# Kernel tuning notes

Hardware: AMD Instinct MI355X
Metric: run time of the kernel (lower is better)

Reference implementation:

```python
import jax, jax.numpy as jnp
import numpy as np

N = 25000      # nodes
E = 300000     # edges
IN = 32        # in_dim
EDF = 16       # edge_feat_dim
HID = 256      # hidden_dim (per-head dim, concat=False)
HEADS = 4
ACT = 16       # num_actions
G = 64         # graphs in batch
KW = 1024      # wire-mask query nodes


def setup_inputs() -> dict:
    key = jax.random.key(0)
    ks = jax.random.split(key, 20)
    def rn(k, shape, s=0.1):
        return jax.random.normal(k, shape, jnp.float32) * s
    return {
        "x": jax.random.normal(ks[0], (N, IN), jnp.float32),
        "edge_attr": jax.random.normal(ks[1], (E, EDF), jnp.float32),
        "wire_mask": jax.random.randint(ks[2], (KW,), 0, N, jnp.int32),
        "edge_index": jax.random.randint(ks[3], (2, E), 0, N, jnp.int32),
        "batch": jnp.sort(jax.random.randint(ks[4], (N,), 0, G, jnp.int32)),
        "enc_w1": rn(ks[5], (EDF, 32)),
        "enc_b1": jnp.zeros((32,), jnp.float32),
        "enc_w2": rn(ks[6], (32, IN * IN), 0.05),
        "enc_b2": jnp.zeros((IN * IN,), jnp.float32),
        "root_w": rn(ks[7], (IN, IN)),
        "nn_bias": jnp.zeros((IN,), jnp.float32),
        "gat1_w": rn(ks[8], (IN, HEADS * HID)),
        "gat1_asrc": rn(ks[9], (HEADS, HID)),
        "gat1_adst": rn(ks[10], (HEADS, HID)),
        "gat1_b": jnp.zeros((HID,), jnp.float32),
        "gat2_w": rn(ks[11], (HID, HEADS * HID)),
        "gat2_asrc": rn(ks[12], (HEADS, HID)),
        "gat2_adst": rn(ks[13], (HEADS, HID)),
        "gat2_b": jnp.zeros((HID,), jnp.float32),
        "wire_w": rn(ks[14], (HID, 1)),
        "wire_b": jnp.zeros((1,), jnp.float32),
        "act_w": rn(ks[15], (HID, ACT)),
        "act_b": jnp.zeros((ACT,), jnp.float32),
    }


def _gat(x, src, dst, W, a_src, a_dst, b):
    # PyG GATConv, concat=False (mean over heads), eval mode (no dropout),
    # self-loops already included in (src, dst).
    H, D = a_src.shape
    h = (x @ W).reshape(-1, H, D)                      # [N, H, D]
    es = (h * a_src[None]).sum(-1)                     # [N, H]
    ed = (h * a_dst[None]).sum(-1)                     # [N, H]
    e = jax.nn.leaky_relu(es[src] + ed[dst], negative_slope=0.2)  # [E2, H]
    m = jax.ops.segment_max(e, dst, num_segments=N)    # segment softmax (stable)
    w = jnp.exp(e - m[dst])
    den = jax.ops.segment_sum(w, dst, num_segments=N)
    alpha = w / (den[dst] + 1e-16)
    out = jax.ops.segment_sum(h[src] * alpha[..., None], dst, num_segments=N)
    return out.mean(axis=1) + b                        # [N, D]


def reference(x, edge_attr, wire_mask, edge_index, batch,
              enc_w1, enc_b1, enc_w2, enc_b2, root_w, nn_bias,
              gat1_w, gat1_asrc, gat1_adst, gat1_b,
              gat2_w, gat2_asrc, gat2_adst, gat2_b,
              wire_w, wire_b, act_w, act_b):
    src, dst = edge_index[0], edge_index[1]
    # NNConv (aggr='mean'): per-edge weight matrix from edge MLP
    We = (jax.nn.relu(edge_attr @ enc_w1 + enc_b1) @ enc_w2 + enc_b2)
    We = We.reshape(E, IN, IN)                         # [E, in, out]
    msg = jnp.einsum('ei,eio->eo', x[src], We)         # [E, out]
    s = jax.ops.segment_sum(msg, dst, num_segments=N)
    cnt = jax.ops.segment_sum(jnp.ones((E,), x.dtype), dst, num_segments=N)
    agg = s / jnp.maximum(cnt, 1.0)[:, None]
    h0 = jax.nn.relu(agg + x @ root_w + nn_bias)
    # GATConv default add_self_loops=True
    sl = jnp.arange(N, dtype=src.dtype)
    src2 = jnp.concatenate([src, sl])
    dst2 = jnp.concatenate([dst, sl])
    h1 = jax.nn.relu(_gat(h0, src2, dst2, gat1_w, gat1_asrc, gat1_adst, gat1_b))
    h2 = jax.nn.relu(_gat(h1, src2, dst2, gat2_w, gat2_asrc, gat2_adst, gat2_b))
    p_wire = (h2[wire_mask] @ wire_w + wire_b).squeeze(-1)   # [KW]
    pooled_s = jax.ops.segment_sum(h2, batch, num_segments=G)
    gc = jax.ops.segment_sum(jnp.ones((N,), h2.dtype), batch, num_segments=G)
    pooled = pooled_s / jnp.maximum(gc, 1.0)[:, None]        # global_mean_pool
    p_action = pooled @ act_w + act_b                        # [G, ACT]
    return (p_wire, p_action)
```

## Files before the change

### kernel.cpp

```cpp
#include <hip/hip_runtime.h>
#include <hip/hip_fp16.h>

#define N_NODES 25000
#define M_PAD   25024
#define N_TILES 1564
#define N_EDGES 300000
#define IN_DIM  32
#define EDFD    16
#define HIDD    256
#define HEADS   4
#define NACT    16
#define NGRAPH  64
#define KWIRE   1024
#define POOL_NB 64

typedef _Float16 half8v __attribute__((ext_vector_type(8)));
typedef __attribute__((ext_vector_type(4))) float f32x4;

__device__ __forceinline__ float leaky(float v) { return v > 0.f ? v : 0.2f * v; }

__global__ __launch_bounds__(256) void k_deg2(const int* __restrict__ ei,
                                              int* __restrict__ deg,
                                              int* __restrict__ deg2) {
    int e = blockIdx.x * 256 + threadIdx.x;
    if (e >= N_EDGES) return;
    atomicAdd(&deg[ei[N_EDGES + e]], 1);
    atomicAdd(&deg2[ei[e]], 1);
}

__global__ __launch_bounds__(256) void k_scan2(const int* __restrict__ degA, int* __restrict__ rpA,
                                               const int* __restrict__ degB, int* __restrict__ rpB) {
    const int* deg = blockIdx.x ? degB : degA;
    int* rowptr    = blockIdx.x ? rpB : rpA;
    __shared__ int part[256];
    int t = threadIdx.x;
    const int CH = 98;
    int base = t * CH;
    int s = 0;
    for (int i = 0; i < CH; ++i) {
        int idx = base + i;
        if (idx < N_NODES) s += deg[idx];
    }
    part[t] = s;
    __syncthreads();
    if (t == 0) {
        int run = 0;
        for (int i = 0; i < 256; ++i) { int v = part[i]; part[i] = run; run += v; }
    }
    __syncthreads();
    int run = part[t];
    for (int i = 0; i < CH; ++i) {
        int idx = base + i;
        if (idx < N_NODES) { rowptr[idx] = run; run += deg[idx]; }
    }
    if (N_NODES >= base && N_NODES < base + CH) rowptr[N_NODES] = run;
}

__global__ __launch_bounds__(256) void k_scatter2(const int* __restrict__ ei,
                                                  const float* __restrict__ ea,
                                                  const int* __restrict__ rowptr,
                                                  const int* __restrict__ rowptr2,
                                                  int* __restrict__ cursor,
                                                  int* __restrict__ cursor2,
                                                  int* __restrict__ csrc,
                                                  int* __restrict__ cdst,
                                                  int* __restrict__ posMap,
                                                  __half* __restrict__ eaP) {
    int e = blockIdx.x * 256 + threadIdx.x;
    if (e >= N_EDGES) return;
    int src = ei[e], dst = ei[N_EDGES + e];
    int p1 = atomicAdd(&cursor[dst], 1);
    int r1 = rowptr[dst] + p1;
    csrc[r1] = src;
    int p2 = atomicAdd(&cursor2[src], 1);
    int r2 = rowptr2[src] + p2;
    cdst[r2] = dst;
    posMap[r2] = r1;
    const float4* src4 = (const float4*)(ea + (size_t)e * EDFD);
    __half2* dp = (__half2*)(eaP + (size_t)r2 * EDFD);
    #pragma unroll
    for (int q = 0; q < EDFD / 4; ++q) {
        float4 v = src4[q];
        dp[q * 2]     = __float22half2_rn(make_float2(v.x, v.y));
        dp[q * 2 + 1] = __float22half2_rn(make_float2(v.z, v.w));
    }
}

__global__ __launch_bounds__(256) void k_prep(const float* __restrict__ w2,
                                              const float* __restrict__ W1,
                                              const float* __restrict__ W2,
                                              const float* __restrict__ a1s,
                                              const float* __restrict__ a1d,
                                              const float* __restrict__ a2s,
                                              const float* __restrict__ a2d,
                                              const float* __restrict__ x,
                                              const float* __restrict__ b2,
                                              const float* __restrict__ w1,
                                              __half* __restrict__ wtt,
                                              __half* __restrict__ wb1,
                                              __half* __restrict__ wb2,
                                              float* __restrict__ wa1,
                                              float* __restrict__ wd1,
                                              float* __restrict__ wa2,
                                              float* __restrict__ wd2,
                                              __half* __restrict__ xf,
                                              float* __restrict__ xb,
                                              __half* __restrict__ w1t) {
    int bid = blockIdx.x, t = threadIdx.x;
    if (bid < 128) {
        int idx = bid * 256 + t;
        int co = idx >> 5, i = idx & 31;
        wtt[idx] = __float2half(w2[(co >> 5) * 1024 + i * 32 + (co & 31)]);
    } else if (bid < 256) {
        int idx = (bid - 128) * 256 + t;
        int d = idx >> 7, k = idx & 127;
        int h = k >> 5, i = k & 31;
        wb1[idx] = __float2half(0.25f * W1[i * 1024 + h * 256 + d]);
    } else if (bid < 1280) {
        int idx = (bid - 256) * 256 + t;
        int d = idx >> 10, k = idx & 1023;
        int h = k >> 8, i = k & 255;
        wb2[idx] = __float2half(0.25f * W2[i * 1024 + h * 256 + d]);
    } else if (bid < 4405) {
        int idx = (bid - 1280) * 256 + t;
        if (idx >= N_NODES * 32) return;
        int n = idx >> 5, o = idx & 31;
        xf[idx] = __float2half(x[idx]);
        float s = 0.f;
        for (int i = 0; i < 32; ++i) s += x[n * 32 + i] * b2[i * 32 + o];
        xb[idx] = s;
    } else if (bid == 4405) {
        if (t >= 128) return;
        int h = t >> 5, i = t & 31;
        float s = 0.f, sd = 0.f;
        for (int d = 0; d < 256; ++d) {
            float w = W1[i * 1024 + h * 256 + d];
            s  += w * a1s[h * 256 + d];
            sd += w * a1d[h * 256 + d];
        }
        wa1[t] = s; wd1[t] = sd;
    } else if (bid < 4410) {
        int idx = (bid - 4406) * 256 + t;
        if (idx >= 1024) return;
        int h = idx >> 8, i = idx & 255;
        float s = 0.f, sd = 0.f;
        for (int d = 0; d < 256; ++d) {
            float w = W2[i * 1024 + h * 256 + d];
            s  += w * a2s[h * 256 + d];
            sd += w * a2d[h * 256 + d];
        }
        wa2[idx] = s; wd2[idx] = sd;
    } else {
        int idx = (bid - 4410) * 256 + t;
        if (idx >= 32 * EDFD) return;
        int j = idx >> 4, k = idx & 15;
        w1t[idx] = __float2half(w1[k * 32 + j]);
    }
}

__global__ __launch_bounds__(256) void k_msg3(const int* __restrict__ rowptr2,
                                              const int* __restrict__ posMap,
                                              const __half* __restrict__ eaP,
                                              const __half* __restrict__ w1t,
                                              const float* __restrict__ b1,
                                              const __half* __restrict__ T,
                                              const float* __restrict__ xb,
                                              __half* __restrict__ msgE) {
    int wv = threadIdx.x >> 6, lane = threadIdx.x & 63;
    int src = blockIdx.x * 4 + wv;
    if (src >= N_NODES) return;
    int r0 = rowptr2[src], r1 = rowptr2[src + 1];
    if (r0 == r1) return;
    int lr = lane & 15, lk = (lane >> 4) * 8;

    half8v bf0, bf1;
    const __half* Tp = T + (size_t)src * 1024;
    #pragma unroll
    for (int q = 0; q < 8; ++q) {
        bf0[q] = (_Float16)__half2float(Tp[(lk + q) * 32 + lr]);
        bf1[q] = (_Float16)__half2float(Tp[(lk + q) * 32 + 16 + lr]);
    }

    __half2 w1r[8][EDFD / 2];
    #pragma unroll
    for (int q = 0; q < 8; ++q) {
        const __half2* wp = (const __half2*)(w1t + (lk + q) * EDFD);
        #pragma unroll
        for (int k2 = 0; k2 < EDFD / 2; ++k2) w1r[q][k2] = wp[k2];
    }
    float b1r[8];
    #pragma unroll
    for (int q = 0; q < 8; ++q) b1r[q] = b1[lk + q];

    float xb0 = xb[src * 32 + lr], xb1 = xb[src * 32 + 16 + lr];
    int rbase = (lane >> 4) * 4;

    for (int t0 = r0; t0 < r1; t0 += 16) {
        int e = t0 + lr;
        bool ok = (e < r1);
        half8v afr;
        if (ok) {
            const __half2* ep = (const __half2*)(eaP + (size_t)e * EDFD);
            __half2 ea2[EDFD / 2];
            #pragma unroll
            for (int k2 = 0; k2 < EDFD / 2; ++k2) ea2[k2] = ep[k2];
            #pragma unroll
            for (int q = 0; q < 8; ++q) {
                float s = b1r[q];
                #pragma unroll
                for (int k2 = 0; k2 < EDFD / 2; ++k2) {
                    float2 v = __half22float2(ea2[k2]);
                    float2 w = __half22float2(w1r[q][k2]);
                    s += v.x * w.x + v.y * w.y;
                }
                afr[q] = (_Float16)fmaxf(s, 0.f);
            }
        } else {
            #pragma unroll
            for (int q = 0; q < 8; ++q) afr[q] = (_Float16)0.f;
        }
        f32x4 c0 = {0.f, 0.f, 0.f, 0.f}, c1 = {0.f, 0.f, 0.f, 0.f};
        c0 = __builtin_amdgcn_mfma_f32_16x16x32_f16(afr, bf0, c0, 0, 0, 0);
        c1 = __builtin_amdgcn_mfma_f32_16x16x32_f16(afr, bf1, c1, 0, 0, 0);
        #pragma unroll
        for (int r = 0; r < 4; ++r) {
            int er = t0 + rbase + r;
            if (er < r1) {
                int pm = posMap[er];
                msgE[(size_t)pm * 32 + lr]      = __float2half(c0[r] + xb0);
                msgE[(size_t)pm * 32 + 16 + lr] = __float2half(c1[r] + xb1);
            }
        }
    }
}

__global__ __launch_bounds__(256) void k_h0e(const float* __restrict__ x,
                                             const float* __restrict__ root_w,
                                             const float* __restrict__ nn_bias,
                                             const __half* __restrict__ msgE,
                                             const int* __restrict__ rowptr,
                                             const float* __restrict__ wa,
                                             const float* __restrict__ wd,
                                             __half* __restrict__ h0f,
                                             float* __restrict__ es,
                                             float* __restrict__ ed) {
    int t = threadIdx.x;
    int ng = t >> 5, o = t & 31;
    int n = blockIdx.x * 8 + ng;
    if (n >= N_NODES) return;
    float s = nn_bias[o];
    for (int k = 0; k < IN_DIM; ++k) s += x[n * IN_DIM + k] * root_w[k * 32 + o];
    int r0 = rowptr[n], r1 = rowptr[n + 1];
    float aggv = 0.f;
    for (int r = r0; r < r1; ++r)
        aggv += __half2float(msgE[(size_t)r * 32 + o]);
    float c = fmaxf((float)(r1 - r0), 1.f);
    s += aggv / c;
    float v = fmaxf(s, 0.f);
    h0f[n * IN_DIM + o] = __float2half(v);
    #pragma unroll
    for (int h = 0; h < 4; ++h) {
        float ss = v * wa[h * 32 + o];
        float dd = v * wd[h * 32 + o];
        #pragma unroll
        for (int off = 16; off; off >>= 1) {
            ss += __shfl_down(ss, off, 32);
            dd += __shfl_down(dd, off, 32);
        }
        if (o == 0) { es[n * 4 + h] = ss; ed[n * 4 + h] = dd; }
    }
}

__global__ __launch_bounds__(256, 2) void k_gemT(const __half* __restrict__ A,
                                                 const __half* __restrict__ Wt,
                                                 __half* __restrict__ C) {
    __shared__ __half cst[4][16 * 36];
    int t = threadIdx.x, wid = t >> 6, lane = t & 63;
    int lr = lane & 15, lk = (lane >> 4) * 8;

    int bid = blockIdx.x;
    int xcd = bid & 7, j = bid >> 3;
    int sx = j & 31;
    int y = ((j >> 5) << 3) | xcd;
    int n0 = sx * 32;

    half8v bfr[2];
    #pragma unroll
    for (int c = 0; c < 2; ++c)
        bfr[c] = *(const half8v*)(Wt + (size_t)(n0 + c * 16 + lr) * 32 + lk);

    int tb = (y * 4 + wid) * 4;
    for (int pp = 0; pp < 4; pp += 2) {
        int tA = tb + pp;
        if (tA >= N_TILES) break;
        int mA = tA * 16, mB = mA + 16;
        half8v aA = *(const half8v*)(A + (size_t)(mA + lr) * 32 + lk);
        half8v aB = *(const half8v*)(A + (size_t)(mB + lr) * 32 + lk);
        f32x4 acc[2][2];
        #pragma unroll
        for (int i = 0; i < 2; ++i)
            #pragma unroll
            for (int c = 0; c < 2; ++c)
                acc[i][c] = (f32x4){0.f, 0.f, 0.f, 0.f};
        acc[0][0] = __builtin_amdgcn_mfma_f32_16x16x32_f16(aA, bfr[0], acc[0][0], 0, 0, 0);
        acc[0][1] = __builtin_amdgcn_mfma_f32_16x16x32_f16(aA, bfr[1], acc[0][1], 0, 0, 0);
        acc[1][0] = __builtin_amdgcn_mfma_f32_16x16x32_f16(aB, bfr[0], acc[1][0], 0, 0, 0);
        acc[1][1] = __builtin_amdgcn_mfma_f32_16x16x32_f16(aB, bfr[1], acc[1][1], 0, 0, 0);

        int rbase = (lane >> 4) * 4;
        #pragma unroll
        for (int ti = 0; ti < 2; ++ti) {
            #pragma unroll
            for (int c = 0; c < 2; ++c)
                #pragma unroll
                for (int r = 0; r < 4; ++r)
                    cst[wid][(rbase + r) * 36 + c * 16 + lr] = __float2half(acc[ti][c][r]);
            int m0 = ti ? mB : mA;
            #pragma unroll
            for (int p = 0; p < 2; ++p) {
                int row = p * 8 + (lane >> 3), hb = lane & 7;
                float2 v = *(const float2*)((const char*)&cst[wid][0] + row * 72 + hb * 8);
                *(float2*)((char*)C + ((size_t)(m0 + row) * 1024 + n0) * 2 + hb * 8) = v;
            }
        }
    }
}

template <int K, typename OT, bool FUSE_ED>
__global__ __launch_bounds__(256, 3) void k_gemmo(const __half* __restrict__ A,
                                                  const __half* __restrict__ Wt,
                                                  const float* __restrict__ bias,
                                                  OT* __restrict__ C,
                                                  const float* __restrict__ wa,
                                                  const float* __restrict__ wd,
                                                  float* __restrict__ es,
                                                  float* __restrict__ ed) {
    constexpr int CK  = 128;
    constexpr int KC  = K / CK;
    constexpr int KSC = CK / 32;
    constexpr int CB  = CK * 2;
    __shared__ __half bs[2][64 * CK];
    __shared__ float cst[4][16 * 36];
    int t = threadIdx.x, wid = t >> 6, lane = t & 63;
    int lr = lane & 15, lk = (lane >> 4) * 8;

    int bid = blockIdx.x;
    int xcd = bid & 7, rest = bid >> 3;
    int strip = rest & 3, yhi = rest >> 2;
    int y = yhi * 8 + xcd;
    if (y >= 196) return;
    int n0 = strip * 64;
    float bv[4];
    #pragma unroll
    for (int c = 0; c < 4; ++c) bv[c] = bias[n0 + c * 16 + lr];
    int tb = y * 8 + wid * 2;
    int tA0 = tb     < N_TILES ? tb     : N_TILES - 1;
    int tA1 = tb + 1 < N_TILES ? tb + 1 : N_TILES - 1;
    const int swz = (lr & 7) << 4;

    f32x4 acc[2][4];
    #pragma unroll
    for (int i = 0; i < 2; ++i)
        #pragma unroll
        for (int c = 0; c < 4; ++c)
            acc[i][c] = (f32x4){0.f, 0.f, 0.f, 0.f};

    #define STAGE_CHUNK(BUF, KCN)                                                              \
        _Pragma("unroll")                                                                      \
        for (int it = 0; it < (64 * CB) / (256 * 16); ++it) {                                  \
            int lo = it * 4096 + wid * 1024 + lane * 16;                                       \
            int col = lo >> 8;                                                                 \
            int go = lo ^ ((col & 7) << 4);                                                    \
            const char* sp_ = (const char*)Wt + ((size_t)(n0 + col) * K + (KCN) * CK) * 2      \
                              + (go & (CB - 1));                                               \
            __builtin_amdgcn_global_load_lds(                                                  \
                (const __attribute__((address_space(1))) void*)sp_,                            \
                (__attribute__((address_space(3))) void*)((char*)bs[BUF] + it * 4096 + wid * 1024), \
                16, 0, 0);                                                                     \
        }

    STAGE_CHUNK(0, 0)
    __syncthreads();

    const __half* pA0 = A + (size_t)(tA0 * 16 + lr) * K + lk;
    const __half* pA1 = A + (size_t)(tA1 * 16 + lr) * K + lk;

    for (int kc = 0; kc < KC; ++kc) {
        int cur = kc & 1;
        if (kc + 1 < KC) {
            STAGE_CHUNK(cur ^ 1, kc + 1)
        }
        half8v aH0[KSC], aH1[KSC];
        #pragma unroll
        for (int ks = 0; ks < KSC; ++ks) {
            aH0[ks] = *(const half8v*)(pA0 + kc * CK + ks * 32);
            aH1[ks] = *(const half8v*)(pA1 + kc * CK + ks * 32);
        }
        #pragma unroll
        for (int ks = 0; ks < KSC; ++ks) {
            #pragma unroll
            for (int c = 0; c < 4; ++c) {
                half8v b = *(const half8v*)((const char*)bs[cur] +
                            (((c * 16 + lr) * CB + lk * 2 + ks * 64) ^ swz));
                acc[0][c] = __builtin_amdgcn_mfma_f32_16x16x32_f16(aH0[ks], b, acc[0][c], 0, 0, 0);
                acc[1][c] = __builtin_amdgcn_mfma_f32_16x16x32_f16(aH1[ks], b, acc[1][c], 0, 0, 0);
            }
        }
        if (kc + 1 < KC) __syncthreads();
    }
    #undef STAGE_CHUNK

    int rbase = (lane >> 4) * 4;
    #pragma unroll
    for (int ti = 0; ti < 2; ++ti) {
        if (tb + ti >= N_TILES) break;
        int m0 = (tb + ti) * 16;
        int row = lane >> 2, cg = lane & 3;
        #pragma unroll
        for (int half = 0; half < 2; ++half) {
            #pragma unroll
            for (int c = 0; c < 2; ++c)
                #pragma unroll
                for (int r = 0; r < 4; ++r)
                    cst[wid][(rbase + r) * 36 + c * 16 + lr] =
                        fmaxf(acc[ti][half * 2 + c][r] + bv[half * 2 + c], 0.f);
            int colb = n0 + half * 32;
            const float* sp = &cst[wid][row * 36 + cg * 8];
            if constexpr (sizeof(OT) == 2) {
                __half2 o0 = __float22half2_rn(make_float2(sp[0], sp[1]));
                __half2 o1 = __float22half2_rn(make_float2(sp[2], sp[3]));
                __half2 o2 = __float22half2_rn(make_float2(sp[4], sp[5]));
                __half2 o3 = __float22half2_rn(make_float2(sp[6], sp[7]));
                float4 v = make_float4(__uint_as_float(*(unsigned*)&o0), __uint_as_float(*(unsigned*)&o1),
                                       __uint_as_float(*(unsigned*)&o2), __uint_as_float(*(unsigned*)&o3));
                *(float4*)((__half*)C + (size_t)(m0 + row) * 256 + colb + cg * 8) = v;
            } else {
                float4 v0 = make_float4(sp[0], sp[1], sp[2], sp[3]);
                float4 v1 = make_float4(sp[4], sp[5], sp[6], sp[7]);
                float* cp = (float*)C + (size_t)(m0 + row) * 256 + colb + cg * 8;
                *(float4*)cp = v0;
                *(float4*)(cp + 4) = v1;
            }
            if constexpr (FUSE_ED) {
                int rowg = m0 + row;
                #pragma unroll
                for (int h = 0; h < 4; ++h) {
                    float pes = 0.f, ped = 0.f;
                    #pragma unroll
                    for (int d = 0; d < 8; ++d) {
                        float vv = sp[d];
                        pes += vv * wa[h * 256 + colb + cg * 8 + d];
                        ped += vv * wd[h * 256 + colb + cg * 8 + d];
                    }
                    pes += __shfl_down(pes, 1, 4); pes += __shfl_down(pes, 2, 4);
                    ped += __shfl_down(ped, 1, 4); ped += __shfl_down(ped, 2, 4);
                    if (cg == 0 && rowg < N_NODES) {
                        atomicAdd(&es[rowg * 4 + h], pes);
                        atomicAdd(&ed[rowg * 4 + h], ped);
                    }
                }
            }
        }
    }
}

__global__ __launch_bounds__(256) void k_agg1(const int* __restrict__ rowptr,
                                              const int* __restrict__ csrc,
                                              const float* __restrict__ es,
                                              const float* __restrict__ ed,
                                              const __half* __restrict__ h0f,
                                              __half* __restrict__ agg0) {
    int dst = blockIdx.x * 4 + (threadIdx.x >> 6);
    if (dst >= N_NODES) return;
    int lane = threadIdx.x & 63;
    int h = lane >> 4, i2 = lane & 15;
    float edv = ed[dst * 4 + h];
    float vself = leaky(es[dst * 4 + h] + edv);
    float dn = 1.f;
    int r0 = rowptr[dst], r1 = rowptr[dst + 1];

    __half2 hv = *(const __half2*)(h0f + (size_t)dst * 32 + i2 * 2);
    float2 f = __half22float2(hv);
    float ax = f.x, ay = f.y;
    for (int r = r0; r < r1; ++r) {
        int src = csrc[r];
        float w = __expf(leaky(es[src * 4 + h] + edv) - vself);
        dn += w;
        __half2 sv = *(const __half2*)(h0f + (size_t)src * 32 + i2 * 2);
        float2 g = __half22float2(sv);
        ax += w * g.x; ay += w * g.y;
    }
    float inv = 1.f / (dn + 1e-16f);
    *(__half2*)(agg0 + (size_t)dst * 128 + h * 32 + i2 * 2) =
        __float22half2_rn(make_float2(ax * inv, ay * inv));
}

__global__ __launch_bounds__(256) void k_agg2(const int* __restrict__ rowptr,
                                              const int* __restrict__ csrc,
                                              const float* __restrict__ es,
                                              const float* __restrict__ ed,
                                              const __half* __restrict__ h1f,
                                              __half* __restrict__ agg1) {
    int dst = blockIdx.x * 4 + (threadIdx.x >> 6);
    if (dst >= N_NODES) return;
    int lane = threadIdx.x & 63;
    float vs[4], edv[4], dn[4];
    float acc[4][4];
    {
        float2 q = *(const float2*)(h1f + (size_t)dst * 256 + lane * 4);
        const __half2* hq = (const __half2*)&q;
        float2 f0 = __half22float2(hq[0]), f1 = __half22float2(hq[1]);
        #pragma unroll
        for (int h = 0; h < 4; ++h) {
            edv[h] = ed[dst * 4 + h];
            vs[h] = leaky(es[dst * 4 + h] + edv[h]);
            dn[h] = 1.f;
            acc[h][0] = f0.x; acc[h][1] = f0.y;
            acc[h][2] = f1.x; acc[h][3] = f1.y;
        }
    }
    int r0 = rowptr[dst], r1 = rowptr[dst + 1];
    for (int r = r0; r < r1; ++r) {
        int src = csrc[r];
        float4 esv = *(const float4*)(es + (size_t)src * 4);
        float w0 = __expf(leaky(esv.x + edv[0]) - vs[0]);
        float w1 = __expf(leaky(esv.y + edv[1]) - vs[1]);
        float w2 = __expf(leaky(esv.z + edv[2]) - vs[2]);
        float w3 = __expf(leaky(esv.w + edv[3]) - vs[3]);
        dn[0] += w0; dn[1] += w1; dn[2] += w2; dn[3] += w3;
        float2 q = *(const float2*)(h1f + (size_t)src * 256 + lane * 4);
        const __half2* hq = (const __half2*)&q;
        float2 f0 = __half22float2(hq[0]), f1 = __half22float2(hq[1]);
        acc[0][0] += w0 * f0.x; acc[0][1] += w0 * f0.y; acc[0][2] += w0 * f1.x; acc[0][3] += w0 * f1.y;
        acc[1][0] += w1 * f0.x; acc[1][1] += w1 * f0.y; acc[1][2] += w1 * f1.x; acc[1][3] += w1 * f1.y;
        acc[2][0] += w2 * f0.x; acc[2][1] += w2 * f0.y; acc[2][2] += w2 * f1.x; acc[2][3] += w2 * f1.y;
        acc[3][0] += w3 * f0.x; acc[3][1] += w3 * f0.y; acc[3][2] += w3 * f1.x; acc[3][3] += w3 * f1.y;
    }
    #pragma unroll
    for (int h = 0; h < 4; ++h) {
        float inv = 1.f / (dn[h] + 1e-16f);
        __half2 o0 = __float22half2_rn(make_float2(acc[h][0] * inv, acc[h][1] * inv));
        __half2 o1 = __float22half2_rn(make_float2(acc[h][2] * inv, acc[h][3] * inv));
        __half2* op = (__half2*)(agg1 + (size_t)dst * 1024 + h * 256 + lane * 4);
        op[0] = o0; op[1] = o1;
    }
}

__global__ __launch_bounds__(256) void k_wirepool(const int* __restrict__ wm,
                                                  const float* __restrict__ h2,
                                                  const float* __restrict__ ww,
                                                  const float* __restrict__ wb,
                                                  const int* __restrict__ batch,
                                                  float* __restrict__ out,
                                                  float* __restrict__ pooled,
                                                  float* __restrict__ gcnt) {
    int bid = blockIdx.x;
    if (bid < KWIRE / 4) {
        int k = bid * 4 + (threadIdx.x >> 6);
        int lane = threadIdx.x & 63;
        int n = wm[k];
        float s = 0.f;
        for (int d = lane; d < 256; d += 64) s += h2[(size_t)n * 256 + d] * ww[d];
        #pragma unroll
        for (int off = 32; off; off >>= 1) s += __shfl_down(s, off);
        if (lane == 0) out[k] = s + wb[0];
        return;
    }
    int n0 = (bid - KWIRE / 4) * POOL_NB;
    int n1 = n0 + POOL_NB; if (n1 > N_NODES) n1 = N_NODES;
    int d = threadIdx.x;
    int cur = batch[n0];
    float acc = 0.f, cnt = 0.f;
    for (int n = n0; n < n1; ++n) {
        int g = batch[n];
        if (g != cur) {
            atomicAdd(&pooled[cur * 256 + d], acc);
            if (d == 0) atomicAdd(&gcnt[cur], cnt);
            acc = 0.f; cnt = 0.f; cur = g;
        }
        acc += h2[(size_t)n * 256 + d];
        cnt += 1.f;
    }
    atomicAdd(&pooled[cur * 256 + d], acc);
    if (d == 0) atomicAdd(&gcnt[cur], cnt);
}

__global__ __launch_bounds__(256) void k_act(const float* __restrict__ pooled,
                                             const float* __restrict__ gcnt,
                                             const float* __restrict__ aw,
                                             const float* __restrict__ ab,
                                             float* __restrict__ out) {
    int u = blockIdx.x * 4 + (threadIdx.x >> 6);
    int lane = threadIdx.x & 63;
    if (u >= NGRAPH * NACT) return;
    int g = u >> 4, a = u & 15;
    float c = fmaxf(gcnt[g], 1.f);
    float s = 0.f;
    for (int d = lane; d < 256; d += 64) s += pooled[g * 256 + d] * aw[d * 16 + a];
    #pragma unroll
    for (int off = 32; off; off >>= 1) s += __shfl_down(s, off);
    if (lane == 0) out[KWIRE + u] = s / c + ab[a];
}

extern "C" void kernel_launch(void* const* d_in, const int* in_sizes, int n_in,
                              void* d_out, int out_size, void* d_ws, size_t ws_size,
                              hipStream_t stream) {
    const float* x        = (const float*)d_in[0];
    const float* edge_attr= (const float*)d_in[1];
    const int*   wire_mask= (const int*)d_in[2];
    const int*   edge_idx = (const int*)d_in[3];
    const int*   batch    = (const int*)d_in[4];
    const float* enc_w1   = (const float*)d_in[5];
    const float* enc_b1   = (const float*)d_in[6];
    const float* enc_w2   = (const float*)d_in[7];
    const float* enc_b2   = (const float*)d_in[8];
    const float* root_w   = (const float*)d_in[9];
    const float* nn_bias  = (const float*)d_in[10];
    const float* gat1_w   = (const float*)d_in[11];
    const float* gat1_asrc= (const float*)d_in[12];
    const float* gat1_adst= (const float*)d_in[13];
    const float* gat1_b   = (const float*)d_in[14];
    const float* gat2_w   = (const float*)d_in[15];
    const float* gat2_asrc= (const float*)d_in[16];
    const float* gat2_adst= (const float*)d_in[17];
    const float* gat2_b   = (const float*)d_in[18];
    const float* wire_w   = (const float*)d_in[19];
    const float* wire_b   = (const float*)d_in[20];
    const float* act_w    = (const float*)d_in[21];
    const float* act_b    = (const float*)d_in[22];
    float* out = (float*)d_out;

    float* ws = (float*)d_ws;
    size_t off = 0;
    __half* T16   = (__half*)(ws + off); off += (size_t)M_PAD * 1024 / 2;
    __half* agg1f = (__half*)(ws + off); off += (size_t)M_PAD * 1024 / 2;
    __half* agg0f = (__half*)(ws + off); off += (size_t)M_PAD * 128 / 2;
    __half* h0f   = (__half*)(ws + off); off += (size_t)M_PAD * 32 / 2;
    __half* h1f   = (__half*)(ws + off); off += (size_t)M_PAD * 256 / 2;
    __half* xf    = (__half*)(ws + off); off += (size_t)M_PAD * 32 / 2;
    __half* eaP   = (__half*)(ws + off); off += (size_t)N_EDGES * EDFD / 2;
    __half* msgE  = (__half*)(ws + off); off += (size_t)N_EDGES * 32 / 2;
    float* xb     = ws + off; off += 800000;
    float* esb    = ws + off; off += 100000;
    float* edb    = ws + off; off += 100000;
    float* h2     = ws + off; off += (size_t)M_PAD * 256;
    float* pooled = ws + off; off += NGRAPH * 256;
    float* gcnt   = ws + off; off += NGRAPH;
    int* deg      = (int*)(ws + off); off += 25600;
    int* deg2     = (int*)(ws + off); off += 25600;
    int* cursor   = (int*)(ws + off); off += 25600;
    int* cursor2  = (int*)(ws + off); off += 25600;
    int* rowptr   = (int*)(ws + off); off += 25600;
    int* rowptr2  = (int*)(ws + off); off += 25600;
    int* csrc     = (int*)(ws + off); off += N_EDGES;
    int* cdst     = (int*)(ws + off); off += N_EDGES;
    int* posMap   = (int*)(ws + off); off += N_EDGES;
    __half* wtt   = (__half*)(ws + off); off += 16384;
    __half* wb1t  = (__half*)(ws + off); off += 16384;
    __half* wb2t  = (__half*)(ws + off); off += 131072;
    __half* w1t   = (__half*)(ws + off); off += 256;
    float* wa1    = ws + off; off += 128;
    float* wd1    = ws + off; off += 128;
    float* wa2    = ws + off; off += 1024;
    float* wd2    = ws + off; off += 1024;
    float* esb2   = ws + off; off += 100000;
    float* edb2   = ws + off; off += 100000;

    const int GBT = 3328;
    const int GBO = 800;

    hipMemsetAsync(deg, 0, 4 * 25600 * sizeof(int), stream);
    hipMemsetAsync(esb2, 0, 2 * 100000 * sizeof(float), stream);
    k_deg2<<<(N_EDGES + 255) / 256, 256, 0, stream>>>(edge_idx, deg, deg2);
    k_scan2<<<2, 256, 0, stream>>>(deg, rowptr, deg2, rowptr2);
    k_scatter2<<<(N_EDGES + 255) / 256, 256, 0, stream>>>(edge_idx, edge_attr, rowptr, rowptr2,
                                                          cursor, cursor2, csrc, cdst, posMap, eaP);

    k_prep<<<4412, 256, 0, stream>>>(enc_w2, gat1_w, gat2_w, gat1_asrc, gat1_adst,
                                     gat2_asrc, gat2_adst, x, enc_b2, enc_w1,
                                     wtt, wb1t, wb2t, wa1, wd1, wa2, wd2, xf, xb, w1t);

    k_gemT<<<GBT, 256, 0, stream>>>(xf, wtt, T16);
    k_msg3<<<(N_NODES + 3) / 4, 256, 0, stream>>>(rowptr2, posMap, eaP,
                                                  w1t, enc_b1, T16, xb, msgE);
    k_h0e<<<(N_NODES + 7) / 8, 256, 0, stream>>>(x, root_w, nn_bias, msgE, rowptr,
                                                 wa1, wd1, h0f, esb, edb);

    k_agg1<<<(N_NODES + 3) / 4, 256, 0, stream>>>(rowptr, csrc, esb, edb, h0f, agg0f);
    k_gemmo<128, __half, true><<<GBO, 256, 0, stream>>>(agg0f, wb1t, gat1_b, h1f,
                                                        wa2, wd2, esb2, edb2);

    k_agg2<<<(N_NODES + 3) / 4, 256, 0, stream>>>(rowptr, csrc, esb2, edb2, h1f, agg1f);
    k_gemmo<1024, float, false><<<GBO, 256, 0, stream>>>(agg1f, wb2t, gat2_b, h2,
                                                         nullptr, nullptr, nullptr, nullptr);

    hipMemsetAsync(pooled, 0, (NGRAPH * 256 + NGRAPH) * sizeof(float), stream);
    k_wirepool<<<KWIRE / 4 + (N_NODES + POOL_NB - 1) / POOL_NB, 256, 0, stream>>>(
        wire_mask, h2, wire_w, wire_b, batch, out, pooled, gcnt);
    k_act<<<NGRAPH * NACT / 4, 256, 0, stream>>>(pooled, gcnt, act_w, act_b, out);
}
```

Measured before the change: 412.7 us.

## Precompute GAT attention weights per edge in a separate kernel before aggregation

Adds a k_wgt kernel that computes the exponentiated attention weight for every (edge, head) once and stores it along with the inverse softmax denominator. The aggregation kernels then read these precomputed weights instead of recomputing exp/leaky-relu redundantly in every lane of a wave. The cost is an extra kernel launch per GAT layer, a 4.8 MB weight buffer write and read, and a weight-computing kernel with one thread per (node, head) that walks irregular-length rows.

```diff
diff --git a/kernel.cpp b/kernel.cpp
--- a/kernel.cpp
+++ b/kernel.cpp
@@ -464,19 +464,37 @@
     }
 }
 
+__global__ __launch_bounds__(256) void k_wgt(const int* __restrict__ rowptr,
+                                             const int* __restrict__ csrc,
+                                             const float* __restrict__ es,
+                                             const float* __restrict__ ed,
+                                             float* __restrict__ wgt,
+                                             float* __restrict__ invdn) {
+    int u = blockIdx.x * 256 + threadIdx.x;
+    if (u >= N_NODES * 4) return;
+    int dst = u >> 2, h = u & 3;
+    float edv = ed[u];
+    float vself = leaky(es[u] + edv);
+    float dn = 1.f;
+    int r0 = rowptr[dst], r1 = rowptr[dst + 1];
+    for (int r = r0; r < r1; ++r) {
+        float w = __expf(leaky(es[csrc[r] * 4 + h] + edv) - vself);
+        dn += w;
+        wgt[(size_t)r * 4 + h] = w;
+    }
+    invdn[u] = 1.f / (dn + 1e-16f);
+}
+
 __global__ __launch_bounds__(256) void k_agg1(const int* __restrict__ rowptr,
                                               const int* __restrict__ csrc,
-                                              const float* __restrict__ es,
-                                              const float* __restrict__ ed,
+                                              const float* __restrict__ wgt,
+                                              const float* __restrict__ invdn,
                                               const __half* __restrict__ h0f,
                                               __half* __restrict__ agg0) {
     int dst = blockIdx.x * 4 + (threadIdx.x >> 6);
     if (dst >= N_NODES) return;
     int lane = threadIdx.x & 63;
     int h = lane >> 4, i2 = lane & 15;
-    float edv = ed[dst * 4 + h];
-    float vself = leaky(es[dst * 4 + h] + edv);
-    float dn = 1.f;
     int r0 = rowptr[dst], r1 = rowptr[dst + 1];
 
     __half2 hv = *(const __half2*)(h0f + (size_t)dst * 32 + i2 * 2);
@@ -484,27 +502,25 @@
     float ax = f.x, ay = f.y;
     for (int r = r0; r < r1; ++r) {
         int src = csrc[r];
-        float w = __expf(leaky(es[src * 4 + h] + edv) - vself);
-        dn += w;
+        float w = wgt[(size_t)r * 4 + h];
         __half2 sv = *(const __half2*)(h0f + (size_t)src * 32 + i2 * 2);
         float2 g = __half22float2(sv);
         ax += w * g.x; ay += w * g.y;
     }
-    float inv = 1.f / (dn + 1e-16f);
+    float inv = invdn[dst * 4 + h];
     *(__half2*)(agg0 + (size_t)dst * 128 + h * 32 + i2 * 2) =
         __float22half2_rn(make_float2(ax * inv, ay * inv));
 }
 
 __global__ __launch_bounds__(256) void k_agg2(const int* __restrict__ rowptr,
                                               const int* __restrict__ csrc,
-                                              const float* __restrict__ es,
-                                              const float* __restrict__ ed,
+                                              const float* __restrict__ wgt,
+                                              const float* __restrict__ invdn,
                                               const __half* __restrict__ h1f,
                                               __half* __restrict__ agg1) {
     int dst = blockIdx.x * 4 + (threadIdx.x >> 6);
     if (dst >= N_NODES) return;
     int lane = threadIdx.x & 63;
-    float vs[4], edv[4], dn[4];
     float acc[4][4];
     {
         float2 q = *(const float2*)(h1f + (size_t)dst * 256 + lane * 4);
@@ -512,9 +528,6 @@
         float2 f0 = __half22float2(hq[0]), f1 = __half22float2(hq[1]);
         #pragma unroll
         for (int h = 0; h < 4; ++h) {
-            edv[h] = ed[dst * 4 + h];
-            vs[h] = leaky(es[dst * 4 + h] + edv[h]);
-            dn[h] = 1.f;
             acc[h][0] = f0.x; acc[h][1] = f0.y;
             acc[h][2] = f1.x; acc[h][3] = f1.y;
         }
@@ -522,23 +535,18 @@
     int r0 = rowptr[dst], r1 = rowptr[dst + 1];
     for (int r = r0; r < r1; ++r) {
         int src = csrc[r];
-        float4 esv = *(const float4*)(es + (size_t)src * 4);
-        float w0 = __expf(leaky(esv.x + edv[0]) - vs[0]);
-        float w1 = __expf(leaky(esv.y + edv[1]) - vs[1]);
-        float w2 = __expf(leaky(esv.z + edv[2]) - vs[2]);
-        float w3 = __expf(leaky(esv.w + edv[3]) - vs[3]);
-        dn[0] += w0; dn[1] += w1; dn[2] += w2; dn[3] += w3;
+        float4 wv = *(const float4*)(wgt + (size_t)r * 4);
         float2 q = *(const float2*)(h1f + (size_t)src * 256 + lane * 4);
         const __half2* hq = (const __half2*)&q;
         float2 f0 = __half22float2(hq[0]), f1 = __half22float2(hq[1]);
-        acc[0][0] += w0 * f0.x; acc[0][1] += w0 * f0.y; acc[0][2] += w0 * f1.x; acc[0][3] += w0 * f1.y;
-        acc[1][0] += w1 * f0.x; acc[1][1] += w1 * f0.y; acc[1][2] += w1 * f1.x; acc[1][3] += w1 * f1.y;
-        acc[2][0] += w2 * f0.x; acc[2][1] += w2 * f0.y; acc[2][2] += w2 * f1.x; acc[2][3] += w2 * f1.y;
-        acc[3][0] += w3 * f0.x; acc[3][1] += w3 * f0.y; acc[3][2] += w3 * f1.x; acc[3][3] += w3 * f1.y;
+        acc[0][0] += wv.x * f0.x; acc[0][1] += wv.x * f0.y; acc[0][2] += wv.x * f1.x; acc[0][3] += wv.x * f1.y;
+        acc[1][0] += wv.y * f0.x; acc[1][1] += wv.y * f0.y; acc[1][2] += wv.y * f1.x; acc[1][3] += wv.y * f1.y;
+        acc[2][0] += wv.z * f0.x; acc[2][1] += wv.z * f0.y; acc[2][2] += wv.z * f1.x; acc[2][3] += wv.z * f1.y;
+        acc[3][0] += wv.w * f0.x; acc[3][1] += wv.w * f0.y; acc[3][2] += wv.w * f1.x; acc[3][3] += wv.w * f1.y;
     }
     #pragma unroll
     for (int h = 0; h < 4; ++h) {
-        float inv = 1.f / (dn[h] + 1e-16f);
+        float inv = invdn[dst * 4 + h];
         __half2 o0 = __float22half2_rn(make_float2(acc[h][0] * inv, acc[h][1] * inv));
         __half2 o1 = __float22half2_rn(make_float2(acc[h][2] * inv, acc[h][3] * inv));
         __half2* op = (__half2*)(agg1 + (size_t)dst * 1024 + h * 256 + lane * 4);
@@ -665,9 +673,12 @@
     float* wd2    = ws + off; off += 1024;
     float* esb2   = ws + off; off += 100000;
     float* edb2   = ws + off; off += 100000;
+    float* wgt    = ws + off; off += (size_t)N_EDGES * 4;
+    float* invdn  = ws + off; off += 100000;
 
     const int GBT = 3328;
     const int GBO = 800;
+    const int GW  = (N_NODES * 4 + 255) / 256;
 
     hipMemsetAsync(deg, 0, 4 * 25600 * sizeof(int), stream);
     hipMemsetAsync(esb2, 0, 2 * 100000 * sizeof(float), stream);
@@ -686,11 +697,13 @@
     k_h0e<<<(N_NODES + 7) / 8, 256, 0, stream>>>(x, root_w, nn_bias, msgE, rowptr,
                                                  wa1, wd1, h0f, esb, edb);
 
-    k_agg1<<<(N_NODES + 3) / 4, 256, 0, stream>>>(rowptr, csrc, esb, edb, h0f, agg0f);
+    k_wgt<<<GW, 256, 0, stream>>>(rowptr, csrc, esb, edb, wgt, invdn);
+    k_agg1<<<(N_NODES + 3) / 4, 256, 0, stream>>>(rowptr, csrc, wgt, invdn, h0f, agg0f);
     k_gemmo<128, __half, true><<<GBO, 256, 0, stream>>>(agg0f, wb1t, gat1_b, h1f,
                                                         wa2, wd2, esb2, edb2);
 
-    k_agg2<<<(N_NODES + 3) / 4, 256, 0, stream>>>(rowptr, csrc, esb2, edb2, h1f, agg1f);
+    k_wgt<<<GW, 256, 0, stream>>>(rowptr, csrc, esb2, edb2, wgt, invdn);
+    k_agg2<<<(N_NODES + 3) / 4, 256, 0, stream>>>(rowptr, csrc, wgt, invdn, h1f, agg1f);
     k_gemmo<1024, float, false><<<GBO, 256, 0, stream>>>(agg1f, wb2t, gat2_b, h2,
                                                          nullptr, nullptr, nullptr, nullptr);
 
```

After: 425.9 us. 3.2% more time.
